# Kernel optimization log

Hardware: AMD Instinct MI355X
Metric: run time of the kernel (lower is better)

The kernel has to match this reference:

```python
import jax, jax.numpy as jnp
import numpy as np

NUM_HEADS = 8
LOGIT_MAX = float(np.log(1.0 / 0.01))  # log(100)


def setup_inputs() -> dict:
    key = jax.random.key(0)
    kq, kk, kv, kp = jax.random.split(key, 4)
    B, n, L, C = 16, 100, 64, 256
    return {
        "query": jax.random.normal(kq, (B, n, L, C), dtype=jnp.float32),
        "key": jax.random.normal(kk, (B, n, L, C), dtype=jnp.float32),
        "value": jax.random.normal(kv, (B, n, L, C), dtype=jnp.float32),
        "position": jax.random.normal(kp, (B, NUM_HEADS, L, L), dtype=jnp.float32),
        "logit_scale": jnp.full((NUM_HEADS, 1, 1), np.log(10.0), dtype=jnp.float32),
    }


def reference(query, key, value, position, logit_scale):
    B, n, Lq, C = query.shape
    Lv = key.shape[2]
    H = NUM_HEADS
    Dh = C // H
    q = query.reshape(B, n, Lq, H, Dh)
    k = key.reshape(B, n, Lv, H, Dh)
    v = value.reshape(B, n, Lv, H, Dh)
    # [B, n, H, Lq, Lv]
    attn = jnp.einsum("bnqhd,bnkhd->bnhqk", q, k)
    scale = jnp.exp(jnp.minimum(logit_scale, LOGIT_MAX))  # (H,1,1)
    attn = attn * scale + position[:, None]  # broadcast over window dim n
    attn = jax.nn.softmax(attn, axis=-1)
    x = jnp.einsum("bnhqk,bnkhd->bnqhd", attn, v).reshape(B, n, Lq, C)
    return (x, attn)
```

## Files before the change

### kernel.cpp

```cpp
#include <hip/hip_runtime.h>


typedef __attribute__((ext_vector_type(8))) short bf16x8;
typedef __attribute__((ext_vector_type(4))) float f32x4;

#define LOGIT_MAX_F 4.605170185988091f

__device__ __forceinline__ short f2bf(float f) {
    union { float f; unsigned u; } c; c.f = f;
    unsigned r = c.u + 0x7FFFu + ((c.u >> 16) & 1u);
    return (short)(r >> 16);
}
__device__ __forceinline__ float bf2f(short s) {
    union { unsigned u; float f; } c; c.u = ((unsigned)(unsigned short)s) << 16;
    return c.f;
}

#define KHI_OFF 0
#define KLO_OFF 2560
#define VT_OFF  5120
#define P_OFF   7424
#define SMEM_SHORTS 12032

__global__ __launch_bounds__(256, 5) void tat_attn_kernel(
    const float* __restrict__ Qg, const float* __restrict__ Kg,
    const float* __restrict__ Vg, const float* __restrict__ Pg,
    const float* __restrict__ LSg,
    float* __restrict__ Xout, float* __restrict__ Aout)
{
    constexpr int L = 64, C = 256, H = 8, NW = 100;
    __shared__ short smem[SMEM_SHORTS];

    const int blk = blockIdx.x;
    const int h  = blk & 7;
    const int bw = blk >> 3;
    const int t  = threadIdx.x;
    const int wave = t >> 6;
    const int lane = t & 63;
    const int quad = lane >> 4;
    const int l15  = lane & 15;

    const float* qb = Qg + (size_t)bw * L * C + h * 32;
    const float* kb = Kg + (size_t)bw * L * C + h * 32;
    const float* vb = Vg + (size_t)bw * L * C + h * 32;
    const int b = bw / NW;
    const float* pb = Pg + (size_t)(b * H + h) * L * L;
    float* xb = Xout + (size_t)bw * L * C + h * 32;
    float* ab = Aout + ((size_t)bw * H + h) * L * L;

    const float scale = __expf(fminf(LSg[h], LOGIT_MAX_F));

    const int r8 = t >> 2;
    const int c8 = (t & 3) * 8;
    const float4 k0 = *(const float4*)(kb + r8 * C + c8);
    const float4 k1 = *(const float4*)(kb + r8 * C + c8 + 4);

    const float4 v0 = *(const float4*)(vb + lane * C + wave * 8);
    const float4 v1 = *(const float4*)(vb + lane * C + wave * 8 + 4);

    const int qrow = 16 * wave + l15;
    const float4 q0 = *(const float4*)(qb + qrow * C + quad * 8);
    const float4 q1 = *(const float4*)(qb + qrow * C + quad * 8 + 4);

    float posr[4][4];
    #pragma unroll
    for (int r = 0; r < 4; ++r) {
        const int cb = (16 * wave + quad * 4 + r) * L + l15;
        posr[0][r] = pb[cb + 0];
        posr[1][r] = pb[cb + 16];
        posr[2][r] = pb[cb + 32];
        posr[3][r] = pb[cb + 48];
    }

    {
        const float ka[8] = {k0.x,k0.y,k0.z,k0.w,k1.x,k1.y,k1.z,k1.w};
        bf16x8 kh, kl;
        #pragma unroll
        for (int i = 0; i < 8; ++i) {
            const short hi = f2bf(ka[i]);
            kh[i] = hi;
            kl[i] = f2bf(ka[i] - bf2f(hi));
        }
        *(bf16x8*)(smem + KHI_OFF + r8 * 40 + c8) = kh;
        *(bf16x8*)(smem + KLO_OFF + r8 * 40 + c8) = kl;
    }

    {
        const float va[8] = {v0.x,v0.y,v0.z,v0.w,v1.x,v1.y,v1.z,v1.w};
        #pragma unroll
        for (int i = 0; i < 8; ++i)
            smem[VT_OFF + (wave * 8 + i) * 72 + lane] = f2bf(va[i]);
    }

    bf16x8 qh, ql;
    {
        const float qa[8] = {q0.x,q0.y,q0.z,q0.w,q1.x,q1.y,q1.z,q1.w};
        #pragma unroll
        for (int i = 0; i < 8; ++i) {
            const short hi = f2bf(qa[i]);
            qh[i] = hi;
            ql[i] = f2bf(qa[i] - bf2f(hi));
        }
    }

    __syncthreads();

    f32x4 acc0 = {0,0,0,0}, acc1 = {0,0,0,0}, acc2 = {0,0,0,0}, acc3 = {0,0,0,0};
    #pragma unroll
    for (int t4 = 0; t4 < 4; ++t4) {
        const bf16x8 bkh = *(const bf16x8*)(smem + KHI_OFF + (16*t4 + l15)*40 + quad*8);
        const bf16x8 bkl = *(const bf16x8*)(smem + KLO_OFF + (16*t4 + l15)*40 + quad*8);
        f32x4 a = (t4==0)?acc0:(t4==1)?acc1:(t4==2)?acc2:acc3;
        a = __builtin_amdgcn_mfma_f32_16x16x32_bf16(qh, bkh, a, 0, 0, 0);
        a = __builtin_amdgcn_mfma_f32_16x16x32_bf16(qh, bkl, a, 0, 0, 0);
        a = __builtin_amdgcn_mfma_f32_16x16x32_bf16(ql, bkh, a, 0, 0, 0);
        if (t4==0) acc0 = a; else if (t4==1) acc1 = a; else if (t4==2) acc2 = a; else acc3 = a;
    }

    float lg[4][4];
    #pragma unroll
    for (int r = 0; r < 4; ++r) {
        lg[0][r] = fmaf(acc0[r], scale, posr[0][r]);
        lg[1][r] = fmaf(acc1[r], scale, posr[1][r]);
        lg[2][r] = fmaf(acc2[r], scale, posr[2][r]);
        lg[3][r] = fmaf(acc3[r], scale, posr[3][r]);
    }

    float p[4][4];
    #pragma unroll
    for (int r = 0; r < 4; ++r) {
        float m = fmaxf(fmaxf(lg[0][r], lg[1][r]), fmaxf(lg[2][r], lg[3][r]));
        #pragma unroll
        for (int off = 8; off > 0; off >>= 1) m = fmaxf(m, __shfl_xor(m, off));
        const float e0 = __expf(lg[0][r] - m);
        const float e1 = __expf(lg[1][r] - m);
        const float e2 = __expf(lg[2][r] - m);
        const float e3 = __expf(lg[3][r] - m);
        float s = (e0 + e1) + (e2 + e3);
        #pragma unroll
        for (int off = 8; off > 0; off >>= 1) s += __shfl_xor(s, off);
        const float inv = 1.0f / s;
        p[0][r] = e0 * inv; p[1][r] = e1 * inv; p[2][r] = e2 * inv; p[3][r] = e3 * inv;
    }

    #pragma unroll
    for (int r = 0; r < 4; ++r) {
        const int row = 16 * wave + quad * 4 + r;
        #pragma unroll
        for (int t4 = 0; t4 < 4; ++t4) {
            const int col = 16 * t4 + l15;
            ab[row * L + col] = p[t4][r];
            smem[P_OFF + row * 72 + col] = f2bf(p[t4][r]);
        }
    }

    f32x4 o0 = {0,0,0,0}, o1 = {0,0,0,0};
    #pragma unroll
    for (int hh = 0; hh < 2; ++hh) {
        const bf16x8 ap  = *(const bf16x8*)(smem + P_OFF + (16*wave + l15)*72 + hh*32 + quad*8);
        const bf16x8 bv0 = *(const bf16x8*)(smem + VT_OFF + l15*72        + hh*32 + quad*8);
        const bf16x8 bv1 = *(const bf16x8*)(smem + VT_OFF + (l15+16)*72   + hh*32 + quad*8);
        o0 = __builtin_amdgcn_mfma_f32_16x16x32_bf16(ap, bv0, o0, 0, 0, 0);
        o1 = __builtin_amdgcn_mfma_f32_16x16x32_bf16(ap, bv1, o1, 0, 0, 0);
    }

    #pragma unroll
    for (int r = 0; r < 4; ++r) {
        const int row = 16 * wave + quad * 4 + r;
        xb[row * C + l15]      = o0[r];
        xb[row * C + 16 + l15] = o1[r];
    }
}

extern "C" void kernel_launch(void* const* d_in, const int* in_sizes, int n_in,
                              void* d_out, int out_size, void* d_ws, size_t ws_size,
                              hipStream_t stream) {
    const float* q   = (const float*)d_in[0];
    const float* k   = (const float*)d_in[1];
    const float* v   = (const float*)d_in[2];
    const float* pos = (const float*)d_in[3];
    const float* ls  = (const float*)d_in[4];
    float* out = (float*)d_out;

    constexpr int B = 16, NW = 100, L = 64, C = 256, H = 8;
    float* x_out = out;
    float* a_out = out + (size_t)B * NW * L * C;

    const int blocks = B * NW * H;
    tat_attn_kernel<<<blocks, 256, 0, stream>>>(q, k, v, pos, ls, x_out, a_out);
}
```

Before: 545.1 us.

## Process four windows per block with register prefetch of next tile

Each block now handles four consecutive windows for one head instead of one, loading the position bias and scale once and reusing them across all four. Inside a loop, the next window's Q/K/V are prefetched into registers while the current window is computed, so global load latency overlaps with MFMA and softmax work. This cuts the grid by a factor of four and adds two barriers per iteration and more live registers. Since 100 windows divide evenly by four, all four windows in a group share the same batch index and therefore the same position tile.

```diff
diff --git a/kernel.cpp b/kernel.cpp
--- a/kernel.cpp
+++ b/kernel.cpp
@@ -28,147 +28,165 @@
     const float* __restrict__ LSg,
     float* __restrict__ Xout, float* __restrict__ Aout)
 {
-    constexpr int L = 64, C = 256, H = 8, NW = 100;
+    constexpr int L = 64, C = 256, H = 8, NW = 100, NT = 4;
     __shared__ short smem[SMEM_SHORTS];
 
-    const int blk = blockIdx.x;
-    const int h  = blk & 7;
-    const int bw = blk >> 3;
-    const int t  = threadIdx.x;
+    const int blk  = blockIdx.x;
+    const int h    = blk & 7;
+    const int grp  = blk >> 3;
+    const int bw0  = grp * NT;
+    const int t    = threadIdx.x;
     const int wave = t >> 6;
     const int lane = t & 63;
     const int quad = lane >> 4;
     const int l15  = lane & 15;
 
-    const float* qb = Qg + (size_t)bw * L * C + h * 32;
-    const float* kb = Kg + (size_t)bw * L * C + h * 32;
-    const float* vb = Vg + (size_t)bw * L * C + h * 32;
-    const int b = bw / NW;
+    const int b = bw0 / NW;
     const float* pb = Pg + (size_t)(b * H + h) * L * L;
-    float* xb = Xout + (size_t)bw * L * C + h * 32;
-    float* ab = Aout + ((size_t)bw * H + h) * L * L;
-
     const float scale = __expf(fminf(LSg[h], LOGIT_MAX_F));
-
-    const int r8 = t >> 2;
-    const int c8 = (t & 3) * 8;
-    const float4 k0 = *(const float4*)(kb + r8 * C + c8);
-    const float4 k1 = *(const float4*)(kb + r8 * C + c8 + 4);
-
-    const float4 v0 = *(const float4*)(vb + lane * C + wave * 8);
-    const float4 v1 = *(const float4*)(vb + lane * C + wave * 8 + 4);
-
-    const int qrow = 16 * wave + l15;
-    const float4 q0 = *(const float4*)(qb + qrow * C + quad * 8);
-    const float4 q1 = *(const float4*)(qb + qrow * C + quad * 8 + 4);
 
     float posr[4][4];
     #pragma unroll
     for (int r = 0; r < 4; ++r) {
         const int cb = (16 * wave + quad * 4 + r) * L + l15;
-        posr[0][r] = pb[cb + 0];
+        posr[0][r] = pb[cb];
         posr[1][r] = pb[cb + 16];
         posr[2][r] = pb[cb + 32];
         posr[3][r] = pb[cb + 48];
     }
 
-    {
-        const float ka[8] = {k0.x,k0.y,k0.z,k0.w,k1.x,k1.y,k1.z,k1.w};
-        bf16x8 kh, kl;
-        #pragma unroll
-        for (int i = 0; i < 8; ++i) {
-            const short hi = f2bf(ka[i]);
-            kh[i] = hi;
-            kl[i] = f2bf(ka[i] - bf2f(hi));
-        }
-        *(bf16x8*)(smem + KHI_OFF + r8 * 40 + c8) = kh;
-        *(bf16x8*)(smem + KLO_OFF + r8 * 40 + c8) = kl;
-    }
-
-    {
-        const float va[8] = {v0.x,v0.y,v0.z,v0.w,v1.x,v1.y,v1.z,v1.w};
-        #pragma unroll
-        for (int i = 0; i < 8; ++i)
-            smem[VT_OFF + (wave * 8 + i) * 72 + lane] = f2bf(va[i]);
-    }
-
-    bf16x8 qh, ql;
-    {
-        const float qa[8] = {q0.x,q0.y,q0.z,q0.w,q1.x,q1.y,q1.z,q1.w};
-        #pragma unroll
-        for (int i = 0; i < 8; ++i) {
-            const short hi = f2bf(qa[i]);
-            qh[i] = hi;
-            ql[i] = f2bf(qa[i] - bf2f(hi));
-        }
-    }
-
-    __syncthreads();
-
-    f32x4 acc0 = {0,0,0,0}, acc1 = {0,0,0,0}, acc2 = {0,0,0,0}, acc3 = {0,0,0,0};
-    #pragma unroll
-    for (int t4 = 0; t4 < 4; ++t4) {
-        const bf16x8 bkh = *(const bf16x8*)(smem + KHI_OFF + (16*t4 + l15)*40 + quad*8);
-        const bf16x8 bkl = *(const bf16x8*)(smem + KLO_OFF + (16*t4 + l15)*40 + quad*8);
-        f32x4 a = (t4==0)?acc0:(t4==1)?acc1:(t4==2)?acc2:acc3;
-        a = __builtin_amdgcn_mfma_f32_16x16x32_bf16(qh, bkh, a, 0, 0, 0);
-        a = __builtin_amdgcn_mfma_f32_16x16x32_bf16(qh, bkl, a, 0, 0, 0);
-        a = __builtin_amdgcn_mfma_f32_16x16x32_bf16(ql, bkh, a, 0, 0, 0);
-        if (t4==0) acc0 = a; else if (t4==1) acc1 = a; else if (t4==2) acc2 = a; else acc3 = a;
-    }
-
-    float lg[4][4];
-    #pragma unroll
-    for (int r = 0; r < 4; ++r) {
-        lg[0][r] = fmaf(acc0[r], scale, posr[0][r]);
-        lg[1][r] = fmaf(acc1[r], scale, posr[1][r]);
-        lg[2][r] = fmaf(acc2[r], scale, posr[2][r]);
-        lg[3][r] = fmaf(acc3[r], scale, posr[3][r]);
-    }
-
-    float p[4][4];
-    #pragma unroll
-    for (int r = 0; r < 4; ++r) {
-        float m = fmaxf(fmaxf(lg[0][r], lg[1][r]), fmaxf(lg[2][r], lg[3][r]));
-        #pragma unroll
-        for (int off = 8; off > 0; off >>= 1) m = fmaxf(m, __shfl_xor(m, off));
-        const float e0 = __expf(lg[0][r] - m);
-        const float e1 = __expf(lg[1][r] - m);
-        const float e2 = __expf(lg[2][r] - m);
-        const float e3 = __expf(lg[3][r] - m);
-        float s = (e0 + e1) + (e2 + e3);
-        #pragma unroll
-        for (int off = 8; off > 0; off >>= 1) s += __shfl_xor(s, off);
-        const float inv = 1.0f / s;
-        p[0][r] = e0 * inv; p[1][r] = e1 * inv; p[2][r] = e2 * inv; p[3][r] = e3 * inv;
-    }
-
-    #pragma unroll
-    for (int r = 0; r < 4; ++r) {
-        const int row = 16 * wave + quad * 4 + r;
+    const int r8   = t >> 2;
+    const int c8   = (t & 3) * 8;
+    const int qrow = 16 * wave + l15;
+
+    const float* qp = Qg + (size_t)bw0 * L * C + h * 32;
+    const float* kp = Kg + (size_t)bw0 * L * C + h * 32;
+    const float* vp = Vg + (size_t)bw0 * L * C + h * 32;
+    float* xp = Xout + (size_t)bw0 * L * C + h * 32;
+    float* ap = Aout + ((size_t)bw0 * H + h) * L * L;
+
+    float4 kr0 = *(const float4*)(kp + r8 * C + c8);
+    float4 kr1 = *(const float4*)(kp + r8 * C + c8 + 4);
+    float4 vr0 = *(const float4*)(vp + lane * C + wave * 8);
+    float4 vr1 = *(const float4*)(vp + lane * C + wave * 8 + 4);
+    float4 qr0 = *(const float4*)(qp + qrow * C + quad * 8);
+    float4 qr1 = *(const float4*)(qp + qrow * C + quad * 8 + 4);
+
+    #pragma unroll 1
+    for (int j = 0; j < NT; ++j) {
+        __syncthreads();
+
+        {
+            const float ka[8] = {kr0.x,kr0.y,kr0.z,kr0.w,kr1.x,kr1.y,kr1.z,kr1.w};
+            bf16x8 kh, kl;
+            #pragma unroll
+            for (int i = 0; i < 8; ++i) {
+                const short hi = f2bf(ka[i]);
+                kh[i] = hi;
+                kl[i] = f2bf(ka[i] - bf2f(hi));
+            }
+            *(bf16x8*)(smem + KHI_OFF + r8 * 40 + c8) = kh;
+            *(bf16x8*)(smem + KLO_OFF + r8 * 40 + c8) = kl;
+        }
+        {
+            const float va[8] = {vr0.x,vr0.y,vr0.z,vr0.w,vr1.x,vr1.y,vr1.z,vr1.w};
+            #pragma unroll
+            for (int i = 0; i < 8; ++i)
+                smem[VT_OFF + (wave * 8 + i) * 72 + lane] = f2bf(va[i]);
+        }
+        bf16x8 qh, ql;
+        {
+            const float qa[8] = {qr0.x,qr0.y,qr0.z,qr0.w,qr1.x,qr1.y,qr1.z,qr1.w};
+            #pragma unroll
+            for (int i = 0; i < 8; ++i) {
+                const short hi = f2bf(qa[i]);
+                qh[i] = hi;
+                ql[i] = f2bf(qa[i] - bf2f(hi));
+            }
+        }
+
+        if (j + 1 < NT) {
+            const float* kn = kp + (j + 1) * (L * C);
+            const float* vn = vp + (j + 1) * (L * C);
+            const float* qn = qp + (j + 1) * (L * C);
+            kr0 = *(const float4*)(kn + r8 * C + c8);
+            kr1 = *(const float4*)(kn + r8 * C + c8 + 4);
+            vr0 = *(const float4*)(vn + lane * C + wave * 8);
+            vr1 = *(const float4*)(vn + lane * C + wave * 8 + 4);
+            qr0 = *(const float4*)(qn + qrow * C + quad * 8);
+            qr1 = *(const float4*)(qn + qrow * C + quad * 8 + 4);
+        }
+
+        __syncthreads();
+
+        f32x4 acc0 = {0,0,0,0}, acc1 = {0,0,0,0}, acc2 = {0,0,0,0}, acc3 = {0,0,0,0};
         #pragma unroll
         for (int t4 = 0; t4 < 4; ++t4) {
-            const int col = 16 * t4 + l15;
-            ab[row * L + col] = p[t4][r];
-            smem[P_OFF + row * 72 + col] = f2bf(p[t4][r]);
-        }
-    }
-
-    f32x4 o0 = {0,0,0,0}, o1 = {0,0,0,0};
-    #pragma unroll
-    for (int hh = 0; hh < 2; ++hh) {
-        const bf16x8 ap  = *(const bf16x8*)(smem + P_OFF + (16*wave + l15)*72 + hh*32 + quad*8);
-        const bf16x8 bv0 = *(const bf16x8*)(smem + VT_OFF + l15*72        + hh*32 + quad*8);
-        const bf16x8 bv1 = *(const bf16x8*)(smem + VT_OFF + (l15+16)*72   + hh*32 + quad*8);
-        o0 = __builtin_amdgcn_mfma_f32_16x16x32_bf16(ap, bv0, o0, 0, 0, 0);
-        o1 = __builtin_amdgcn_mfma_f32_16x16x32_bf16(ap, bv1, o1, 0, 0, 0);
-    }
-
-    #pragma unroll
-    for (int r = 0; r < 4; ++r) {
-        const int row = 16 * wave + quad * 4 + r;
-        xb[row * C + l15]      = o0[r];
-        xb[row * C + 16 + l15] = o1[r];
+            const bf16x8 bkh = *(const bf16x8*)(smem + KHI_OFF + (16*t4 + l15)*40 + quad*8);
+            const bf16x8 bkl = *(const bf16x8*)(smem + KLO_OFF + (16*t4 + l15)*40 + quad*8);
+            f32x4 a = (t4==0)?acc0:(t4==1)?acc1:(t4==2)?acc2:acc3;
+            a = __builtin_amdgcn_mfma_f32_16x16x32_bf16(qh, bkh, a, 0, 0, 0);
+            a = __builtin_amdgcn_mfma_f32_16x16x32_bf16(qh, bkl, a, 0, 0, 0);
+            a = __builtin_amdgcn_mfma_f32_16x16x32_bf16(ql, bkh, a, 0, 0, 0);
+            if (t4==0) acc0 = a; else if (t4==1) acc1 = a; else if (t4==2) acc2 = a; else acc3 = a;
+        }
+
+        float lg[4][4];
+        #pragma unroll
+        for (int r = 0; r < 4; ++r) {
+            lg[0][r] = fmaf(acc0[r], scale, posr[0][r]);
+            lg[1][r] = fmaf(acc1[r], scale, posr[1][r]);
+            lg[2][r] = fmaf(acc2[r], scale, posr[2][r]);
+            lg[3][r] = fmaf(acc3[r], scale, posr[3][r]);
+        }
+
+        float p[4][4];
+        #pragma unroll
+        for (int r = 0; r < 4; ++r) {
+            float m = fmaxf(fmaxf(lg[0][r], lg[1][r]), fmaxf(lg[2][r], lg[3][r]));
+            #pragma unroll
+            for (int off = 8; off > 0; off >>= 1) m = fmaxf(m, __shfl_xor(m, off));
+            const float e0 = __expf(lg[0][r] - m);
+            const float e1 = __expf(lg[1][r] - m);
+            const float e2 = __expf(lg[2][r] - m);
+            const float e3 = __expf(lg[3][r] - m);
+            float s = (e0 + e1) + (e2 + e3);
+            #pragma unroll
+            for (int off = 8; off > 0; off >>= 1) s += __shfl_xor(s, off);
+            const float inv = 1.0f / s;
+            p[0][r] = e0 * inv; p[1][r] = e1 * inv; p[2][r] = e2 * inv; p[3][r] = e3 * inv;
+        }
+
+        float* xb = xp + j * (L * C);
+        float* ab = ap + (size_t)j * H * L * L;
+
+        #pragma unroll
+        for (int r = 0; r < 4; ++r) {
+            const int row = 16 * wave + quad * 4 + r;
+            #pragma unroll
+            for (int t4 = 0; t4 < 4; ++t4) {
+                const int col = 16 * t4 + l15;
+                ab[row * L + col] = p[t4][r];
+                smem[P_OFF + row * 72 + col] = f2bf(p[t4][r]);
+            }
+        }
+
+        f32x4 o0 = {0,0,0,0}, o1 = {0,0,0,0};
+        #pragma unroll
+        for (int hh = 0; hh < 2; ++hh) {
+            const bf16x8 app = *(const bf16x8*)(smem + P_OFF + (16*wave + l15)*72 + hh*32 + quad*8);
+            const bf16x8 bv0 = *(const bf16x8*)(smem + VT_OFF + l15*72        + hh*32 + quad*8);
+            const bf16x8 bv1 = *(const bf16x8*)(smem + VT_OFF + (l15+16)*72   + hh*32 + quad*8);
+            o0 = __builtin_amdgcn_mfma_f32_16x16x32_bf16(app, bv0, o0, 0, 0, 0);
+            o1 = __builtin_amdgcn_mfma_f32_16x16x32_bf16(app, bv1, o1, 0, 0, 0);
+        }
+
+        #pragma unroll
+        for (int r = 0; r < 4; ++r) {
+            const int row = 16 * wave + quad * 4 + r;
+            xb[row * C + l15]      = o0[r];
+            xb[row * C + 16 + l15] = o1[r];
+        }
     }
 }
 
@@ -182,10 +200,10 @@
     const float* ls  = (const float*)d_in[4];
     float* out = (float*)d_out;
 
-    constexpr int B = 16, NW = 100, L = 64, C = 256, H = 8;
+    constexpr int B = 16, NW = 100, L = 64, C = 256, H = 8, NT = 4;
     float* x_out = out;
     float* a_out = out + (size_t)B * NW * L * C;
 
-    const int blocks = B * NW * H;
+    const int blocks = B * NW * H / NT;
     tat_attn_kernel<<<blocks, 256, 0, stream>>>(q, k, v, pos, ls, x_out, a_out);
 }
```

After: 615.1 us. 1.13x slower.
